# Optimization experiments

Hardware: AMD Instinct MI355X
Metric: run time of the kernel (lower is better)

Reference implementation:

```python
import jax, jax.numpy as jnp
import numpy as np

EMB = 256
HID = 256
NH = 8
HD = HID // NH  # 32
EPS = 1e-5


def _wn(v, g):
    # torch weight_norm(dim=0): per-output-row normalization of v
    return g[:, None] * v / jnp.linalg.norm(v, axis=1, keepdims=True)


def _ln(x, gamma, beta):
    mu = jnp.mean(x, axis=-1, keepdims=True)
    var = jnp.mean((x - mu) ** 2, axis=-1, keepdims=True)
    return (x - mu) * jax.lax.rsqrt(var + EPS) * gamma + beta


def _rope(x):
    # x: [B', S, H, D]; torchtune-style rotary embedding, base 10000
    S, D = x.shape[1], x.shape[3]
    freqs = 1.0 / (10000.0 ** (jnp.arange(0, D, 2, dtype=jnp.float32) / D))  # [D/2]
    ang = jnp.arange(S, dtype=jnp.float32)[:, None] * freqs[None, :]          # [S, D/2]
    cos = jnp.cos(ang)[None, :, None, :]
    sin = jnp.sin(ang)[None, :, None, :]
    xr = x.reshape(*x.shape[:-1], D // 2, 2)
    x0, x1 = xr[..., 0], xr[..., 1]
    out = jnp.stack([x0 * cos - x1 * sin, x1 * cos + x0 * sin], axis=-1)
    return out.reshape(x.shape)


def setup_inputs() -> dict:
    key = jax.random.key(0)
    ks = jax.random.split(key, 12)
    s = lambda shp: 0.02
    return {
        "z": jax.random.normal(ks[0], (2, 32, 512, EMB), dtype=jnp.float32),
        "ln1_g": jnp.ones((EMB,), jnp.float32),
        "ln1_b": jnp.zeros((EMB,), jnp.float32),
        "proj_v": jax.random.normal(ks[1], (3 * HID, EMB), jnp.float32) * 0.02,
        "proj_g": jnp.ones((3 * HID,), jnp.float32),
        "proj_b": jnp.zeros((3 * HID,), jnp.float32),
        "ff_v": jax.random.normal(ks[2], (EMB, HID), jnp.float32) * 0.02,
        "ff_g": jnp.ones((EMB,), jnp.float32),
        "ff_b": jnp.zeros((EMB,), jnp.float32),
        "ln2_g": jnp.ones((EMB,), jnp.float32),
        "ln2_b": jnp.zeros((EMB,), jnp.float32),
        "w1_v": jax.random.normal(ks[3], (EMB, EMB), jnp.float32) * 0.02,
        "w1_g": jnp.ones((EMB,), jnp.float32),
        "w1_b": jnp.zeros((EMB,), jnp.float32),
        "w2_v": jax.random.normal(ks[4], (EMB, EMB), jnp.float32) * 0.02,
        "w2_g": jnp.ones((EMB,), jnp.float32),
        "w2_b": jnp.zeros((EMB,), jnp.float32),
    }


def reference(z, ln1_g, ln1_b, proj_v, proj_g, proj_b, ff_v, ff_g, ff_b,
              ln2_g, ln2_b, w1_v, w1_g, w1_b, w2_v, w2_g, w2_b):
    B, U, A, E = z.shape
    BU = B * U
    Wqkv = _wn(proj_v, proj_g)   # [3H, E]
    Wo = _wn(ff_v, ff_g)         # [E, H]
    # ---- RoPE attention block ----
    z_ = _ln(z, ln1_g, ln1_b).reshape(BU, A, E)
    qkv = z_ @ Wqkv.T + proj_b                       # [BU, A, 3H]
    qkv = qkv.reshape(BU, A, NH, 3 * HD)
    q, k, v = jnp.split(qkv, 3, axis=-1)             # each [BU, A, NH, HD]
    q = _rope(q)
    k = _rope(k)
    qh = q.transpose(0, 2, 1, 3)                     # [BU, NH, A, HD]
    kh = k.transpose(0, 2, 1, 3)
    vh = v.transpose(0, 2, 1, 3)
    scores = jnp.einsum('bhqd,bhkd->bhqk', qh, kh) / jnp.sqrt(jnp.float32(HD))
    attn = jax.nn.softmax(scores, axis=-1)
    out = jnp.einsum('bhqk,bhkd->bhqd', attn, vh)    # [BU, NH, A, HD]
    out = out.transpose(0, 2, 1, 3).reshape(BU, A, HID)
    out = out @ Wo.T + ff_b
    z = z + out.reshape(B, U, A, E)
    # ---- NormFF block ----
    W1 = _wn(w1_v, w1_g)
    W2 = _wn(w2_v, w2_g)
    h = _ln(z, ln2_g, ln2_b)
    h = jax.nn.gelu(h @ W1.T + w1_b, approximate=False)
    h = h @ W2.T + w2_b
    return z + h
```

## Files before the change

kernel.cpp:

```cpp
#include <hip/hip_runtime.h>
#include <cmath>

#define EMB 256
#define NHEAD 8
#define HD 32
#define A_LEN 512
#define TOK 32768

typedef __bf16 bf16_t;
typedef __bf16 bf16x8 __attribute__((ext_vector_type(8)));
typedef __bf16 bf16x4 __attribute__((ext_vector_type(4)));
typedef float floatx4 __attribute__((ext_vector_type(4)));

#define MFMA16(a, b, c) __builtin_amdgcn_mfma_f32_16x16x32_bf16((a), (b), (c), 0, 0, 0)

__device__ __forceinline__ float gelu_f(float x) {
    float ax = fabsf(x) * 0.7071067811865476f;
    float t = __builtin_amdgcn_rcpf(fmaf(0.3275911f, ax, 1.0f));
    float poly = t * fmaf(t, fmaf(t, fmaf(t, fmaf(t, 1.061405429f, -1.453152027f),
                          1.421413741f), -0.284496736f), 0.254829592f);
    float erfv = 1.0f - poly * __expf(-ax * ax);
    erfv = copysignf(erfv, x);
    return 0.5f * x * (1.0f + erfv);
}

__global__ __launch_bounds__(64) void setup_kernel(
    const float* __restrict__ proj_v, const float* __restrict__ proj_g,
    const float* __restrict__ ff_v, const float* __restrict__ ff_g,
    const float* __restrict__ w1_v, const float* __restrict__ w1_g,
    const float* __restrict__ w2_v, const float* __restrict__ w2_g,
    bf16_t* __restrict__ Wall, float* __restrict__ ctab,
    float* __restrict__ stab) {
    int b = blockIdx.x;
    int lane = threadIdx.x;
    if (b < 1536) {
        const float* v; const float* g; int r;
        if (b < 768)       { v = proj_v; g = proj_g; r = b; }
        else if (b < 1024) { v = ff_v;   g = ff_g;   r = b - 768; }
        else if (b < 1280) { v = w1_v;   g = w1_g;   r = b - 1024; }
        else               { v = w2_v;   g = w2_g;   r = b - 1280; }
        const floatx4* vr = (const floatx4*)(v + (size_t)r * 256);
        floatx4 x = vr[lane];
        float ss = x[0] * x[0] + x[1] * x[1] + x[2] * x[2] + x[3] * x[3];
#pragma unroll
        for (int off = 32; off >= 1; off >>= 1) ss += __shfl_xor(ss, off);
        float sc = g[r] * rsqrtf(ss);
        bf16x4 o;
        o[0] = (bf16_t)(x[0] * sc); o[1] = (bf16_t)(x[1] * sc);
        o[2] = (bf16_t)(x[2] * sc); o[3] = (bf16_t)(x[3] * sc);
        ((bf16x4*)(Wall + (size_t)b * 256))[lane] = o;
    } else {
        int idx = (b - 1536) * 64 + lane;
        int a = idx >> 4, i = idx & 15;
        float freq = expf(-(float)(2 * i) * 0.2878231366242558f);
        float ang = (float)a * freq;
        ctab[idx] = cosf(ang);
        stab[idx] = sinf(ang);
    }
}

__global__ __launch_bounds__(256, 4) void qkv_kernel(
    const float* __restrict__ z, const float* __restrict__ ln_g,
    const float* __restrict__ ln_b, const bf16_t* __restrict__ W,
    const float* __restrict__ pb, const float* __restrict__ ctab,
    const float* __restrict__ stab, bf16_t* __restrict__ qbf,
    bf16_t* __restrict__ kbf, bf16_t* __restrict__ vtb) {
    __shared__ bf16_t xns[32 * 264];
    __shared__ bf16_t stg[8704];
    int tid = threadIdx.x;
    int t0 = blockIdx.x * 32;
    int bu = t0 >> 9, a0 = t0 & 511;

#pragma unroll
    for (int it = 0; it < 2; ++it) {
        int row = it * 16 + (tid >> 4);
        int sub = tid & 15;
        const floatx4* zr = (const floatx4*)(z + (size_t)(t0 + row) * 256 + sub * 16);
        floatx4 v0 = zr[0], v1 = zr[1], v2 = zr[2], v3 = zr[3];
        float vals[16];
        ((floatx4*)vals)[0] = v0; ((floatx4*)vals)[1] = v1;
        ((floatx4*)vals)[2] = v2; ((floatx4*)vals)[3] = v3;
        float s = 0.f, q2 = 0.f;
#pragma unroll
        for (int i = 0; i < 16; ++i) { s += vals[i]; q2 += vals[i] * vals[i]; }
#pragma unroll
        for (int off = 8; off >= 1; off >>= 1) {
            s += __shfl_xor(s, off);
            q2 += __shfl_xor(q2, off);
        }
        float mu = s * (1.f / 256.f);
        float inv = rsqrtf(q2 * (1.f / 256.f) - mu * mu + 1e-5f);
        int cb = sub * 16;
        bf16x8 o0, o1;
#pragma unroll
        for (int i = 0; i < 8; ++i)
            o0[i] = (bf16_t)((vals[i] - mu) * inv * ln_g[cb + i] + ln_b[cb + i]);
#pragma unroll
        for (int i = 0; i < 8; ++i)
            o1[i] = (bf16_t)((vals[8 + i] - mu) * inv * ln_g[cb + 8 + i] + ln_b[cb + 8 + i]);
        *(bf16x8*)&xns[row * 264 + cb] = o0;
        *(bf16x8*)&xns[row * 264 + cb + 8] = o1;
    }
    __syncthreads();

    int wv = tid >> 6, lane = tid & 63, quad = lane >> 4, lidx = lane & 15;

#pragma unroll 1
    for (int sec = 0; sec < 2; ++sec) {
        bf16_t* __restrict__ dst = (sec == 0) ? qbf : kbf;
        floatx4 acc[4][2];
#pragma unroll
        for (int ntl = 0; ntl < 4; ++ntl) {
            int cb = wv * 64 + ntl * 16;
            int ht = cb >> 5;
            floatx4 b4 = *(const floatx4*)&pb[ht * 96 + sec * 32 + (cb & 31) + quad * 4];
            acc[ntl][0] = b4; acc[ntl][1] = b4;
        }
#pragma unroll 2
        for (int kc = 0; kc < 8; ++kc) {
            bf16x8 x0 = *(const bf16x8*)&xns[lidx * 264 + kc * 32 + quad * 8];
            bf16x8 x1 = *(const bf16x8*)&xns[(16 + lidx) * 264 + kc * 32 + quad * 8];
#pragma unroll
            for (int ntl = 0; ntl < 4; ++ntl) {
                int cb = wv * 64 + ntl * 16;
                int ht = cb >> 5;
                int n = ht * 96 + sec * 32 + (cb & 31) + lidx;
                bf16x8 wf = *(const bf16x8*)&W[(size_t)n * 256 + kc * 32 + quad * 8];
                acc[ntl][0] = MFMA16(wf, x0, acc[ntl][0]);
                acc[ntl][1] = MFMA16(wf, x1, acc[ntl][1]);
            }
        }
        float scl = (sec == 0) ? 0.17677669529663687f : 1.0f;
#pragma unroll
        for (int ntl = 0; ntl < 4; ++ntl) {
            int cb = wv * 64 + ntl * 16;
            int d0 = (cb & 31) + quad * 4;
            int fi = d0 >> 1;
#pragma unroll
            for (int tt = 0; tt < 2; ++tt) {
                int al = tt * 16 + lidx;
                int a = a0 + al;
                float cs0 = ctab[a * 16 + fi],     cs1 = ctab[a * 16 + fi + 1];
                float sn0 = stab[a * 16 + fi],     sn1 = stab[a * 16 + fi + 1];
                floatx4 v = acc[ntl][tt];
                bf16x4 o;
                o[0] = (bf16_t)((v[0] * cs0 - v[1] * sn0) * scl);
                o[1] = (bf16_t)((v[1] * cs0 + v[0] * sn0) * scl);
                o[2] = (bf16_t)((v[2] * cs1 - v[3] * sn1) * scl);
                o[3] = (bf16_t)((v[3] * cs1 + v[2] * sn1) * scl);
                *(bf16x4*)&stg[al * 264 + cb + quad * 4] = o;
            }
        }
        __syncthreads();
#pragma unroll
        for (int i = 0; i < 4; ++i) {
            int cid = i * 256 + tid;
            int chunk = cid & 3, al = (cid >> 2) & 31, ht = cid >> 7;
            bf16x8 vv = *(const bf16x8*)&stg[al * 264 + ht * 32 + chunk * 8];
            *(bf16x8*)&dst[((size_t)((bu * 8 + ht) * 512 + a0 + al)) * 32 + chunk * 8] = vv;
        }
        __syncthreads();
    }

    {
        floatx4 acc[4][2];
#pragma unroll
        for (int ntl = 0; ntl < 4; ++ntl) {
            int cb = wv * 64 + ntl * 16;
            int ht = cb >> 5;
            float b = pb[ht * 96 + 64 + (cb & 31) + lidx];
            acc[ntl][0] = (floatx4){b, b, b, b};
            acc[ntl][1] = (floatx4){b, b, b, b};
        }
#pragma unroll 2
        for (int kc = 0; kc < 8; ++kc) {
            bf16x8 x0 = *(const bf16x8*)&xns[lidx * 264 + kc * 32 + quad * 8];
            bf16x8 x1 = *(const bf16x8*)&xns[(16 + lidx) * 264 + kc * 32 + quad * 8];
#pragma unroll
            for (int ntl = 0; ntl < 4; ++ntl) {
                int cb = wv * 64 + ntl * 16;
                int ht = cb >> 5;
                int n = ht * 96 + 64 + (cb & 31) + lidx;
                bf16x8 wf = *(const bf16x8*)&W[(size_t)n * 256 + kc * 32 + quad * 8];
                acc[ntl][0] = MFMA16(x0, wf, acc[ntl][0]);
                acc[ntl][1] = MFMA16(x1, wf, acc[ntl][1]);
            }
        }
#pragma unroll
        for (int ntl = 0; ntl < 4; ++ntl) {
            int vcol = wv * 64 + ntl * 16 + lidx;
#pragma unroll
            for (int tt = 0; tt < 2; ++tt)
#pragma unroll
                for (int r = 0; r < 4; ++r)
                    stg[vcol * 34 + tt * 16 + quad * 4 + r] = (bf16_t)acc[ntl][tt][r];
        }
        __syncthreads();
#pragma unroll
        for (int i = 0; i < 4; ++i) {
            int cid = i * 256 + tid;
            int chunk = cid & 3, vcol = cid >> 2;
            bf16x8 vv = *(const bf16x8*)&stg[vcol * 34 + chunk * 8];
            *(bf16x8*)&vtb[((size_t)(bu * 256 + vcol)) * 512 + a0 + chunk * 8] = vv;
        }
    }
}

__global__ __launch_bounds__(512, 4) void attn_kernel(
    const bf16_t* __restrict__ qbf, const bf16_t* __restrict__ kbf,
    const bf16_t* __restrict__ vtb, bf16_t* __restrict__ ob) {
    __shared__ bf16_t Kls[512 * 32];
    __shared__ bf16_t Vt[32 * 512];
    int tid = threadIdx.x;
    int wv = tid >> 6, lane = tid & 63, quad = lane >> 4, lidx = lane & 15;
    int bh = blockIdx.x;
    int bu = bh >> 3, h = bh & 7;
    size_t hb = (size_t)bh * (A_LEN * HD);

#pragma unroll
    for (int i = 0; i < 4; ++i) {
        int c = tid + i * 512;
        int key = c >> 2, blk = c & 3;
        bf16x8 kv = *(const bf16x8*)&kbf[hb + (size_t)c * 8];
        *(bf16x8*)&Kls[key * 32 + ((blk ^ (key & 3)) << 3)] = kv;
        int vrow = c >> 6, vblk = c & 63;
        bf16x8 vv = *(const bf16x8*)&vtb[hb + (size_t)c * 8];
        *(bf16x8*)&Vt[vrow * 512 + ((vblk ^ (vrow & 7)) << 3)] = vv;
    }
    __syncthreads();

    const floatx4 cm8 = (floatx4){-8.f, -8.f, -8.f, -8.f};
    const floatx4 zero4 = (floatx4){0.f, 0.f, 0.f, 0.f};
    int krow = ((lidx >> 2) << 3) + (lidx & 3);
    int kswz = (quad ^ (lidx & 3)) << 3;

#pragma unroll 1
    for (int mt = 0; mt < 4; ++mt) {
        int q0 = wv * 64 + mt * 16;
        bf16x8 qfrag = *(const bf16x8*)&qbf[hb + (size_t)(q0 + lidx) * 32 + quad * 8];
        float l_ = 0.f;
        floatx4 Oacc[2];
        Oacc[0] = zero4; Oacc[1] = zero4;

#pragma unroll 1
        for (int kc = 0; kc < 8; ++kc) {
            floatx4 sc[4];
#pragma unroll
            for (int t = 0; t < 4; ++t) {
                int row = kc * 64 + (t >> 1) * 32 + ((t & 1) << 2) + krow;
                bf16x8 kf = *(const bf16x8*)&Kls[row * 32 + kswz];
                sc[t] = MFMA16(kf, qfrag, cm8);
            }
            float p[4][4];
#pragma unroll
            for (int t = 0; t < 4; ++t)
#pragma unroll
                for (int r = 0; r < 4; ++r) p[t][r] = __expf(sc[t][r]);
#pragma unroll
            for (int t = 0; t < 4; ++t)
                l_ += (p[t][0] + p[t][1]) + (p[t][2] + p[t][3]);
            bf16x8 pa0, pa1;
#pragma unroll
            for (int r = 0; r < 4; ++r) {
                pa0[r]     = (bf16_t)p[0][r];
                pa0[4 + r] = (bf16_t)p[1][r];
                pa1[r]     = (bf16_t)p[2][r];
                pa1[4 + r] = (bf16_t)p[3][r];
            }
#pragma unroll
            for (int nt = 0; nt < 2; ++nt) {
                int vr = nt * 16 + lidx;
                bf16x8 vf0 = *(const bf16x8*)&Vt[vr * 512 +
                    ((kc * 8 + ((0 * 4 + quad) ^ (lidx & 7))) << 3)];
                Oacc[nt] = MFMA16(pa0, vf0, Oacc[nt]);
                bf16x8 vf1 = *(const bf16x8*)&Vt[vr * 512 +
                    ((kc * 8 + ((1 * 4 + quad) ^ (lidx & 7))) << 3)];
                Oacc[nt] = MFMA16(pa1, vf1, Oacc[nt]);
            }
        }

        float s = l_;
        s += __shfl_xor(s, 16);
        s += __shfl_xor(s, 32);
#pragma unroll
        for (int r = 0; r < 4; ++r) {
            float inv = __builtin_amdgcn_rcpf(__shfl(s, quad * 4 + r));
            int tok = bu * 512 + q0 + quad * 4 + r;
#pragma unroll
            for (int nt = 0; nt < 2; ++nt)
                ob[(size_t)tok * 256 + h * 32 + nt * 16 + lidx] =
                    (bf16_t)(Oacc[nt][r] * inv);
        }
    }
}

__global__ __launch_bounds__(256, 4) void tail_kernel(
    const bf16_t* __restrict__ X, const bf16_t* __restrict__ Wo,
    const float* __restrict__ obias, const float* __restrict__ zin,
    const float* __restrict__ ln_g, const float* __restrict__ ln_b,
    const bf16_t* __restrict__ W1, const float* __restrict__ b1,
    const bf16_t* __restrict__ W2, const float* __restrict__ b2,
    float* __restrict__ outp) {
    __shared__ float fbuf[32 * 264];
    __shared__ float red[32 * 8];
    __shared__ float mi[32 * 2];
    bf16_t* xbuf = (bf16_t*)fbuf;
    int tid = threadIdx.x;
    int t0 = blockIdx.x * 32;
    int wv = tid >> 6, lane = tid & 63, quad = lane >> 4, lidx = lane & 15;
    size_t wrow = (size_t)(wv * 64 + lidx) * 256 + quad * 8;

    bf16x8 wfA[4], wfB[4];
#pragma unroll
    for (int nt = 0; nt < 4; ++nt)
        wfA[nt] = *(const bf16x8*)&Wo[wrow + (size_t)nt * 4096];

    {
        int row = tid >> 3;
        int c0 = (tid & 7) * 32;
        const bf16x8* src = (const bf16x8*)&X[(size_t)(t0 + row) * 256 + c0];
        bf16x8* dst = (bf16x8*)&xbuf[row * 264 + c0];
        dst[0] = src[0]; dst[1] = src[1]; dst[2] = src[2]; dst[3] = src[3];
    }
    __syncthreads();

#define GEMM_PIPE(WP, ACC)                                                   \
    do {                                                                     \
        _Pragma("unroll")                                                    \
        for (int kp = 0; kp < 4; ++kp) {                                     \
            _Pragma("unroll")                                                \
            for (int nt = 0; nt < 4; ++nt)                                   \
                wfB[nt] = *(const bf16x8*)&WP[wrow + (size_t)nt * 4096 +     \
                                              kp * 64 + 32];                 \
            bf16x8 a0 = *(const bf16x8*)&xbuf[lidx * 264 + kp * 64 + quad * 8]; \
            bf16x8 a1 = *(const bf16x8*)&xbuf[(16 + lidx) * 264 + kp * 64 + quad * 8]; \
            _Pragma("unroll")                                                \
            for (int nt = 0; nt < 4; ++nt) {                                 \
                ACC[nt][0] = MFMA16(a0, wfA[nt], ACC[nt][0]);                \
                ACC[nt][1] = MFMA16(a1, wfA[nt], ACC[nt][1]);                \
            }                                                                \
            if (kp < 3) {                                                    \
                _Pragma("unroll")                                            \
                for (int nt = 0; nt < 4; ++nt)                               \
                    wfA[nt] = *(const bf16x8*)&WP[wrow + (size_t)nt * 4096 + \
                                                  kp * 64 + 64];             \
            }                                                                \
            a0 = *(const bf16x8*)&xbuf[lidx * 264 + kp * 64 + 32 + quad * 8]; \
            a1 = *(const bf16x8*)&xbuf[(16 + lidx) * 264 + kp * 64 + 32 + quad * 8]; \
            _Pragma("unroll")                                                \
            for (int nt = 0; nt < 4; ++nt) {                                 \
                ACC[nt][0] = MFMA16(a0, wfB[nt], ACC[nt][0]);                \
                ACC[nt][1] = MFMA16(a1, wfB[nt], ACC[nt][1]);                \
            }                                                                \
        }                                                                    \
    } while (0)

    float r1[4][2][4];
    {
        floatx4 acc[4][2];
#pragma unroll
        for (int i = 0; i < 4; ++i) {
            acc[i][0] = (floatx4){0.f, 0.f, 0.f, 0.f};
            acc[i][1] = (floatx4){0.f, 0.f, 0.f, 0.f};
        }
        GEMM_PIPE(Wo, acc);
#pragma unroll
        for (int nt = 0; nt < 4; ++nt) {
            int n = wv * 64 + nt * 16 + lidx;
            float b = obias[n];
#pragma unroll
            for (int mt = 0; mt < 2; ++mt)
#pragma unroll
                for (int r = 0; r < 4; ++r) {
                    size_t o = (size_t)(t0 + mt * 16 + quad * 4 + r) * 256 + n;
                    r1[nt][mt][r] = zin[o] + acc[nt][mt][r] + b;
                }
        }
    }

#pragma unroll
    for (int mt = 0; mt < 2; ++mt)
#pragma unroll
        for (int r = 0; r < 4; ++r) {
            float s = 0.f, ss = 0.f;
#pragma unroll
            for (int nt = 0; nt < 4; ++nt) {
                float v = r1[nt][mt][r];
                s += v; ss += v * v;
            }
#pragma unroll
            for (int off = 8; off >= 1; off >>= 1) {
                s += __shfl_xor(s, off);
                ss += __shfl_xor(ss, off);
            }
            if (lidx == 0) {
                int row = mt * 16 + quad * 4 + r;
                red[row * 8 + wv * 2] = s;
                red[row * 8 + wv * 2 + 1] = ss;
            }
        }
    __syncthreads();
    if (tid < 32) {
        float s = 0.f, ss = 0.f;
#pragma unroll
        for (int w = 0; w < 4; ++w) {
            s += red[tid * 8 + w * 2];
            ss += red[tid * 8 + w * 2 + 1];
        }
        float mu = s * (1.f / 256.f);
        mi[tid * 2] = mu;
        mi[tid * 2 + 1] = rsqrtf(ss * (1.f / 256.f) - mu * mu + 1e-5f);
    }
    __syncthreads();

    {
#pragma unroll
        for (int nt = 0; nt < 4; ++nt)
            wfA[nt] = *(const bf16x8*)&W1[wrow + (size_t)nt * 4096];
        float gv[4], bv[4];
#pragma unroll
        for (int nt = 0; nt < 4; ++nt) {
            int n = wv * 64 + nt * 16 + lidx;
            gv[nt] = ln_g[n]; bv[nt] = ln_b[n];
        }
#pragma unroll
        for (int mt = 0; mt < 2; ++mt)
#pragma unroll
            for (int r = 0; r < 4; ++r) {
                int row = mt * 16 + quad * 4 + r;
                float mu = mi[row * 2], inv = mi[row * 2 + 1];
#pragma unroll
                for (int nt = 0; nt < 4; ++nt) {
                    int n = wv * 64 + nt * 16 + lidx;
                    xbuf[row * 264 + n] =
                        (bf16_t)((r1[nt][mt][r] - mu) * inv * gv[nt] + bv[nt]);
                }
            }
    }
    __syncthreads();

    {
        floatx4 acc[4][2];
#pragma unroll
        for (int i = 0; i < 4; ++i) {
            acc[i][0] = (floatx4){0.f, 0.f, 0.f, 0.f};
            acc[i][1] = (floatx4){0.f, 0.f, 0.f, 0.f};
        }
        GEMM_PIPE(W1, acc);
        __syncthreads();
#pragma unroll
        for (int nt = 0; nt < 4; ++nt)
            wfB[nt] = *(const bf16x8*)&W2[wrow + (size_t)nt * 4096];
#pragma unroll
        for (int nt = 0; nt < 4; ++nt) {
            int n = wv * 64 + nt * 16 + lidx;
            float b = b1[n];
#pragma unroll
            for (int mt = 0; mt < 2; ++mt)
#pragma unroll
                for (int r = 0; r < 4; ++r) {
                    float x = acc[nt][mt][r] + b;
                    xbuf[(mt * 16 + quad * 4 + r) * 264 + n] = (bf16_t)gelu_f(x);
                }
        }
#pragma unroll
        for (int nt = 0; nt < 4; ++nt) wfA[nt] = wfB[nt];
    }
    __syncthreads();

    {
        floatx4 acc[4][2];
#pragma unroll
        for (int i = 0; i < 4; ++i) {
            acc[i][0] = (floatx4){0.f, 0.f, 0.f, 0.f};
            acc[i][1] = (floatx4){0.f, 0.f, 0.f, 0.f};
        }
        GEMM_PIPE(W2, acc);
        __syncthreads();
#pragma unroll
        for (int nt = 0; nt < 4; ++nt) {
            int n = wv * 64 + nt * 16 + lidx;
            float b = b2[n];
#pragma unroll
            for (int mt = 0; mt < 2; ++mt)
#pragma unroll
                for (int r = 0; r < 4; ++r)
                    fbuf[(mt * 16 + quad * 4 + r) * 264 + n] =
                        r1[nt][mt][r] + acc[nt][mt][r] + b;
        }
    }
    __syncthreads();

#pragma unroll
    for (int i = 0; i < 8; ++i) {
        int fid = i * 256 + tid;
        int row = fid >> 6;
        int c4 = (fid & 63) * 4;
        *(floatx4*)&outp[(size_t)(t0 + row) * 256 + c4] =
            *(const floatx4*)&fbuf[row * 264 + c4];
    }
#undef GEMM_PIPE
}

extern "C" void kernel_launch(void* const* d_in, const int* in_sizes, int n_in,
                              void* d_out, int out_size, void* d_ws, size_t ws_size,
                              hipStream_t stream) {
    const float* z      = (const float*)d_in[0];
    const float* ln1_g  = (const float*)d_in[1];
    const float* ln1_b  = (const float*)d_in[2];
    const float* proj_v = (const float*)d_in[3];
    const float* proj_g = (const float*)d_in[4];
    const float* proj_b = (const float*)d_in[5];
    const float* ff_v   = (const float*)d_in[6];
    const float* ff_g   = (const float*)d_in[7];
    const float* ff_b   = (const float*)d_in[8];
    const float* ln2_g  = (const float*)d_in[9];
    const float* ln2_b  = (const float*)d_in[10];
    const float* w1_v   = (const float*)d_in[11];
    const float* w1_g   = (const float*)d_in[12];
    const float* w1_b   = (const float*)d_in[13];
    const float* w2_v   = (const float*)d_in[14];
    const float* w2_g   = (const float*)d_in[15];
    const float* w2_b   = (const float*)d_in[16];
    float* out = (float*)d_out;

    char* p = (char*)d_ws;
    bf16_t* Wall = (bf16_t*)p; p += (size_t)1536 * 256 * 2;
    float* ctab  = (float*)p;  p += 8192 * 4;
    float* stab  = (float*)p;  p += 8192 * 4;
    bf16_t* qbf  = (bf16_t*)p; p += (size_t)TOK * 256 * 2;
    bf16_t* kbf  = (bf16_t*)p; p += (size_t)TOK * 256 * 2;
    bf16_t* vtb  = (bf16_t*)p; p += (size_t)TOK * 256 * 2;
    bf16_t* abuf = (bf16_t*)p; p += (size_t)TOK * 256 * 2;

    const bf16_t* Wqkv = Wall;
    const bf16_t* Wo   = Wall + (size_t)768 * 256;
    const bf16_t* W1   = Wall + (size_t)1024 * 256;
    const bf16_t* W2   = Wall + (size_t)1280 * 256;

    setup_kernel<<<1664, 64, 0, stream>>>(proj_v, proj_g, ff_v, ff_g,
                                          w1_v, w1_g, w2_v, w2_g,
                                          Wall, ctab, stab);
    qkv_kernel<<<TOK / 32, 256, 0, stream>>>(z, ln1_g, ln1_b, Wqkv, proj_b,
                                             ctab, stab, qbf, kbf, vtb);
    attn_kernel<<<64 * 8, 512, 0, stream>>>(qbf, kbf, vtb, abuf);
    tail_kernel<<<TOK / 32, 256, 0, stream>>>(abuf, Wo, ff_b, z, ln2_g, ln2_b,
                                              W1, w1_b, W2, w2_b, out);
}
```

Measured before the change: 245.0 us.

## Halve qkv staging buffer and split epilogue writes to raise occupancy

The shared staging buffer in the QKV kernel is halved, and launch bounds go from 4 to 6 blocks per CU so more blocks fit in LDS. To make the smaller buffer work, the Q/K RoPE epilogue now stages and writes out 16 tokens at a time over two passes. The V-transpose epilogue stages 128 columns at a time, one wave pair per pass. This adds extra __syncthreads, and V is now written to global memory with 4-byte stores instead of 16-byte ones. Tighter register limits may also cause spills.

```diff
diff --git a/kernel.cpp b/kernel.cpp
--- a/kernel.cpp
+++ b/kernel.cpp
@@ -59,14 +59,14 @@
     }
 }
 
-__global__ __launch_bounds__(256, 4) void qkv_kernel(
+__global__ __launch_bounds__(256, 6) void qkv_kernel(
     const float* __restrict__ z, const float* __restrict__ ln_g,
     const float* __restrict__ ln_b, const bf16_t* __restrict__ W,
     const float* __restrict__ pb, const float* __restrict__ ctab,
     const float* __restrict__ stab, bf16_t* __restrict__ qbf,
     bf16_t* __restrict__ kbf, bf16_t* __restrict__ vtb) {
     __shared__ bf16_t xns[32 * 264];
-    __shared__ bf16_t stg[8704];
+    __shared__ __align__(16) bf16_t stg[4352];
     int tid = threadIdx.x;
     int t0 = blockIdx.x * 32;
     int bu = t0 >> 9, a0 = t0 & 511;
@@ -131,35 +131,35 @@
             }
         }
         float scl = (sec == 0) ? 0.17677669529663687f : 1.0f;
-#pragma unroll
-        for (int ntl = 0; ntl < 4; ++ntl) {
-            int cb = wv * 64 + ntl * 16;
-            int d0 = (cb & 31) + quad * 4;
-            int fi = d0 >> 1;
-#pragma unroll
-            for (int tt = 0; tt < 2; ++tt) {
-                int al = tt * 16 + lidx;
-                int a = a0 + al;
+#pragma unroll 1
+        for (int h = 0; h < 2; ++h) {
+#pragma unroll
+            for (int ntl = 0; ntl < 4; ++ntl) {
+                int cb = wv * 64 + ntl * 16;
+                int d0 = (cb & 31) + quad * 4;
+                int fi = d0 >> 1;
+                int a = a0 + h * 16 + lidx;
                 float cs0 = ctab[a * 16 + fi],     cs1 = ctab[a * 16 + fi + 1];
                 float sn0 = stab[a * 16 + fi],     sn1 = stab[a * 16 + fi + 1];
-                floatx4 v = acc[ntl][tt];
+                floatx4 v = acc[ntl][h];
                 bf16x4 o;
                 o[0] = (bf16_t)((v[0] * cs0 - v[1] * sn0) * scl);
                 o[1] = (bf16_t)((v[1] * cs0 + v[0] * sn0) * scl);
                 o[2] = (bf16_t)((v[2] * cs1 - v[3] * sn1) * scl);
                 o[3] = (bf16_t)((v[3] * cs1 + v[2] * sn1) * scl);
-                *(bf16x4*)&stg[al * 264 + cb + quad * 4] = o;
-            }
-        }
-        __syncthreads();
-#pragma unroll
-        for (int i = 0; i < 4; ++i) {
-            int cid = i * 256 + tid;
-            int chunk = cid & 3, al = (cid >> 2) & 31, ht = cid >> 7;
-            bf16x8 vv = *(const bf16x8*)&stg[al * 264 + ht * 32 + chunk * 8];
-            *(bf16x8*)&dst[((size_t)((bu * 8 + ht) * 512 + a0 + al)) * 32 + chunk * 8] = vv;
-        }
-        __syncthreads();
+                *(bf16x4*)&stg[lidx * 264 + cb + quad * 4] = o;
+            }
+            __syncthreads();
+#pragma unroll
+            for (int i = 0; i < 2; ++i) {
+                int cid = i * 256 + tid;
+                int chunk = cid & 3, al = (cid >> 2) & 15, ht = cid >> 6;
+                bf16x8 vv = *(const bf16x8*)&stg[al * 264 + ht * 32 + chunk * 8];
+                *(bf16x8*)&dst[((size_t)((bu * 8 + ht) * 512 + a0 + h * 16 + al)) * 32
+                               + chunk * 8] = vv;
+            }
+            __syncthreads();
+        }
     }
 
     {
@@ -186,22 +186,32 @@
                 acc[ntl][1] = MFMA16(x1, wf, acc[ntl][1]);
             }
         }
-#pragma unroll
-        for (int ntl = 0; ntl < 4; ++ntl) {
-            int vcol = wv * 64 + ntl * 16 + lidx;
-#pragma unroll
-            for (int tt = 0; tt < 2; ++tt)
-#pragma unroll
-                for (int r = 0; r < 4; ++r)
-                    stg[vcol * 34 + tt * 16 + quad * 4 + r] = (bf16_t)acc[ntl][tt][r];
-        }
         __syncthreads();
-#pragma unroll
-        for (int i = 0; i < 4; ++i) {
-            int cid = i * 256 + tid;
-            int chunk = cid & 3, vcol = cid >> 2;
-            bf16x8 vv = *(const bf16x8*)&stg[vcol * 34 + chunk * 8];
-            *(bf16x8*)&vtb[((size_t)(bu * 256 + vcol)) * 512 + a0 + chunk * 8] = vv;
+#pragma unroll 1
+        for (int p = 0; p < 2; ++p) {
+            if ((wv >> 1) == p) {
+#pragma unroll
+                for (int ntl = 0; ntl < 4; ++ntl) {
+                    int vcolL = (wv & 1) * 64 + ntl * 16 + lidx;
+#pragma unroll
+                    for (int tt = 0; tt < 2; ++tt)
+#pragma unroll
+                        for (int r = 0; r < 4; ++r)
+                            stg[vcolL * 34 + tt * 16 + quad * 4 + r] =
+                                (bf16_t)acc[ntl][tt][r];
+                }
+            }
+            __syncthreads();
+#pragma unroll
+            for (int i = 0; i < 8; ++i) {
+                int cid = i * 256 + tid;
+                int vcolL = cid >> 4, dc = cid & 15;
+                unsigned int u = *(const unsigned int*)
+                    ((const char*)stg + vcolL * 68 + dc * 4);
+                *(unsigned int*)&vtb[((size_t)(bu * 256 + p * 128 + vcolL)) * 512
+                                     + a0 + dc * 2] = u;
+            }
+            __syncthreads();
         }
     }
 }
```

Result: slower. 266.7 us (+8.8%).
